# Performance work log

Measured on AMD Instinct MI355X. Metric: run time of the kernel, lower is better.

Reference implementation:

```python
import jax, jax.numpy as jnp
import numpy as np

N_ATOMS = 8192
N_PAIRS = 65536
F = 128        # n_atombasis
R = 20         # n_radialbasis
B = 5          # graph_n_blocks
EPS = 1e-8     # stability constant


def setup_inputs() -> dict:
    key = jax.random.key(0)
    ks = jax.random.split(key, 16)
    rn = lambda k, shape, s=0.05: jax.random.normal(k, shape, dtype=jnp.float32) * s
    return {
        "features": jax.random.normal(ks[0], (N_ATOMS, F), jnp.float32),
        "distances": jax.random.uniform(ks[1], (N_PAIRS,), jnp.float32, 0.5, 5.0),
        "vectors": jax.random.normal(ks[2], (N_PAIRS, 3), jnp.float32),
        "cutoffs": jax.random.uniform(ks[3], (N_PAIRS,), jnp.float32),
        "rbfs": jax.random.normal(ks[4], (N_PAIRS, R), jnp.float32),
        "filter_W": rn(ks[5], (R, B * 3 * F)),
        "filter_b": jnp.zeros((B * 3 * F,), jnp.float32),
        "int_W1": rn(ks[6], (B, F, F)),
        "int_b1": jnp.zeros((B, F), jnp.float32),
        "int_W2": rn(ks[7], (B, F, 3 * F)),
        "int_b2": jnp.zeros((B, 3 * F), jnp.float32),
        "mix_Wv": rn(ks[8], (B, F, 2 * F)),
        "mix_W1": rn(ks[9], (B, 2 * F, F)),
        "mix_b1": jnp.zeros((B, F), jnp.float32),
        "mix_W2": rn(ks[10], (B, F, 3 * F)),
        "mix_b2": jnp.zeros((B, 3 * F), jnp.float32),
        "idx_i": jax.random.randint(ks[11], (N_PAIRS,), 0, N_ATOMS),
        "idx_j": jax.random.randint(ks[12], (N_PAIRS,), 0, N_ATOMS),
    }


def reference(features, distances, vectors, cutoffs, rbfs,
              filter_W, filter_b, int_W1, int_b1, int_W2, int_b2,
              mix_Wv, mix_W1, mix_b1, mix_W2, mix_b2, idx_i, idx_j):
    n_atoms = features.shape[0]
    # Cutoff-weighted radial filters, one (3F) chunk per block: [P, B*3F]
    descriptors = (rbfs @ filter_W + filter_b) * cutoffs[:, None]
    dir_ij = vectors / distances[:, None]                       # [P, 3]

    q = features[:, None, :]                                    # [N, 1, F]
    mu = jnp.zeros((n_atoms, 3, F), dtype=features.dtype)       # [N, 3, F]

    for b in range(B):
        # --- interaction block ---
        x = jax.nn.silu(q @ int_W1[b] + int_b1[b]) @ int_W2[b] + int_b2[b]  # [N,1,3F]
        Wij = descriptors[:, None, b * 3 * F:(b + 1) * 3 * F]               # [P,1,3F]
        xj = x[idx_j] * Wij                                                 # [P,1,3F]
        muj = mu[idx_j]                                                     # [P,3,F]
        dq, dmuR, dmumu = jnp.split(xj, 3, axis=-1)                         # [P,1,F] each
        dmu = dmuR * dir_ij[:, :, None] + dmumu * muj                       # [P,3,F]
        q = q + jax.ops.segment_sum(dq, idx_i, num_segments=n_atoms)
        mu = mu + jax.ops.segment_sum(dmu, idx_i, num_segments=n_atoms)

        # --- mixing block ---
        mu_V, mu_W = jnp.split(mu @ mix_Wv[b], 2, axis=-1)                  # [N,3,F] each
        mu_Vn = jnp.sqrt(jnp.sum(mu_V ** 2, axis=-2, keepdims=True) + EPS)  # [N,1,F]
        ctx = jnp.concatenate([q, mu_Vn], axis=-1)                          # [N,1,2F]
        y = jax.nn.silu(ctx @ mix_W1[b] + mix_b1[b]) @ mix_W2[b] + mix_b2[b]
        dq_i, dmu_i, dqmu_i = jnp.split(y, 3, axis=-1)                      # [N,1,F] each
        q = q + dq_i + dqmu_i * jnp.sum(mu_V * mu_W, axis=1, keepdims=True)
        mu = mu + dmu_i * mu_W

    return q[:, 0, :], mu
```

## Files before the change

### kernel.cpp

```cpp
#include <hip/hip_runtime.h>
#include <hip/hip_bf16.h>

#define NA 8192
#define NP 65536
#define WROW 1920

typedef short short8 __attribute__((ext_vector_type(8)));
typedef short short4v __attribute__((ext_vector_type(4)));
typedef float floatx4 __attribute__((ext_vector_type(4)));

static __device__ __forceinline__ short f2bf(float f) {
    union { float f; unsigned u; } v; v.f = f;
    unsigned r = v.u + 0x7FFF + ((v.u >> 16) & 1);
    return (short)(r >> 16);
}
static __device__ __forceinline__ float bf2f(short s) {
    union { unsigned u; float f; } v;
    v.u = ((unsigned)(unsigned short)s) << 16;
    return v.f;
}
static __device__ __forceinline__ unsigned char f2fp8(float f) {
    int p = __builtin_amdgcn_cvt_pk_fp8_f32(f, 0.f, 0, false);
    return (unsigned char)(p & 0xFF);
}
static __device__ __forceinline__ float fp82f(unsigned char b) {
    return __builtin_amdgcn_cvt_f32_fp8((int)b, 0);
}
static __device__ __forceinline__ float silu(float v) {
    return v / (1.f + __expf(-v));
}

__global__ __launch_bounds__(256) void k_tconv_sw(const float* __restrict__ W,
                                                  short* __restrict__ Wt,
                                                  int K, int N, int total) {
    int idx = blockIdx.x * 256 + threadIdx.x;
    if (idx >= total) return;
    int kn = K * N;
    int b = idx / kn;
    int r = idx - b * kn;
    int tile = r >> 9;
    int li = r & 511;
    int lane = li >> 3, bb = li & 7;
    int Kt = K >> 5;
    int nt = tile / Kt, kt = tile - nt * Kt;
    int k = kt * 32 + (lane >> 4) * 8 + bb;
    int n = nt * 16 + (lane & 15);
    Wt[idx] = f2bf(W[b * kn + k * N + n]);
}

__global__ __launch_bounds__(256) void k_tconv2(const float* __restrict__ fW,
                                                short* __restrict__ fWt) {
    int idx = blockIdx.x * 256 + threadIdx.x;
    if (idx >= 5 * 12288) return;
    int b = idx / 12288;
    int r = idx - b * 12288;
    int nt = r >> 9;
    int li = r & 511;
    int lane = li >> 3, bb = li & 7;
    int k = (lane >> 4) * 8 + bb;
    int n = nt * 16 + (lane & 15);
    fWt[idx] = (k < 20) ? f2bf(fW[k * WROW + b * 384 + n]) : (short)0;
}

__global__ __launch_bounds__(256) void k_init(const float* __restrict__ feat,
                                              float* __restrict__ q,
                                              float* __restrict__ mu,
                                              short* __restrict__ q_bf,
                                              short* __restrict__ mu_bfA,
                                              int* __restrict__ counts,
                                              int* __restrict__ cursor) {
    int idx = blockIdx.x * 256 + threadIdx.x;
    if (idx < NA * 128) { float v = feat[idx]; q[idx] = v; q_bf[idx] = f2bf(v); }
    mu[idx] = 0.f;
    mu_bfA[idx] = 0;
    if (idx < NA) { counts[idx] = 0; cursor[idx] = 0; }
}

__global__ __launch_bounds__(256) void k_hist(const int* __restrict__ idx_i,
                                              int* __restrict__ counts) {
    int p = blockIdx.x * 256 + threadIdx.x;
    if (p < NP) atomicAdd(&counts[idx_i[p]], 1);
}

__global__ __launch_bounds__(1024) void k_scan(const int* __restrict__ counts,
                                               int* __restrict__ offs) {
    __shared__ int sums[1024];
    int t = threadIdx.x;
    int local[8];
    int s = 0;
    #pragma unroll
    for (int k = 0; k < 8; ++k) { local[k] = s; s += counts[t * 8 + k]; }
    sums[t] = s;
    __syncthreads();
    for (int off = 1; off < 1024; off <<= 1) {
        int v = sums[t];
        int u = (t >= off) ? sums[t - off] : 0;
        __syncthreads();
        sums[t] = v + u;
        __syncthreads();
    }
    int base = (t > 0) ? sums[t - 1] : 0;
    #pragma unroll
    for (int k = 0; k < 8; ++k) offs[t * 8 + k] = base + local[k];
    if (t == 1023) offs[NA] = sums[1023];
}

__global__ __launch_bounds__(256) void k_fill(const int* __restrict__ idx_i,
                                              const int* __restrict__ offs,
                                              int* __restrict__ cursor,
                                              int* __restrict__ plist) {
    int p = blockIdx.x * 256 + threadIdx.x;
    if (p < NP) {
        int i = idx_i[p];
        int pos = atomicAdd(&cursor[i], 1);
        plist[offs[i] + pos] = p;
    }
}

__global__ __launch_bounds__(256) void k_prep(const int* __restrict__ plist,
                                              const int* __restrict__ idx_j,
                                              const float* __restrict__ cut,
                                              const float* __restrict__ dist,
                                              const float* __restrict__ vec,
                                              const float* __restrict__ rbfs,
                                              int* __restrict__ jcsr,
                                              float* __restrict__ cut_csr,
                                              float4* __restrict__ dir_csr,
                                              short* __restrict__ rbf_c) {
    int e = blockIdx.x * 256 + threadIdx.x;
    if (e >= NP) {
        if (e < NP + 16) {
            cut_csr[e] = 0.f;
            #pragma unroll
            for (int k = 0; k < 32; ++k) rbf_c[e * 32 + k] = 0;
        }
        return;
    }
    int p = plist[e];
    jcsr[e] = idx_j[p];
    float c = cut[p];
    cut_csr[e] = c;
    float invd = 1.f / dist[p];
    float4 d;
    d.x = vec[p * 3 + 0] * invd;
    d.y = vec[p * 3 + 1] * invd;
    d.z = vec[p * 3 + 2] * invd;
    d.w = 0.f;
    dir_csr[e] = d;
    #pragma unroll
    for (int k = 0; k < 20; ++k) rbf_c[e * 32 + k] = f2bf(rbfs[p * 20 + k] * c);
    #pragma unroll
    for (int k = 20; k < 32; ++k) rbf_c[e * 32 + k] = 0;
}

__global__ __launch_bounds__(256) void k_x(const short* __restrict__ q_bf,
                                           const short* __restrict__ W1sw,
                                           const short* __restrict__ W2sw,
                                           const float* __restrict__ b1,
                                           const float* __restrict__ b2,
                                           unsigned char* __restrict__ x_fp8) {
    __shared__ __align__(16) short qtile[16 * 136];
    __shared__ __align__(16) short hs[16 * 136];
    int t = threadIdx.x;
    int wv = t >> 6, lane = t & 63, quad = lane >> 4, l16 = lane & 15;
    int a0 = blockIdx.x * 16;

    #pragma unroll
    for (int it = 0; it < 2; ++it) {
        int c = it * 256 + t;
        int row = c >> 5, col4 = c & 31;
        *(short4v*)(qtile + row * 136 + col4 * 4) =
            *(const short4v*)(q_bf + (a0 + row) * 128 + col4 * 4);
    }
    __syncthreads();

    floatx4 acc0 = {0.f, 0.f, 0.f, 0.f}, acc1 = {0.f, 0.f, 0.f, 0.f};
    #pragma unroll
    for (int kk = 0; kk < 4; ++kk) {
        short8 a  = *(const short8*)(qtile + l16 * 136 + kk * 32 + quad * 8);
        short8 b0 = *(const short8*)(W1sw + ((wv * 2 + 0) * 4 + kk) * 512 + lane * 8);
        short8 bq = *(const short8*)(W1sw + ((wv * 2 + 1) * 4 + kk) * 512 + lane * 8);
        acc0 = __builtin_amdgcn_mfma_f32_16x16x32_bf16(a, b0, acc0, 0, 0, 0);
        acc1 = __builtin_amdgcn_mfma_f32_16x16x32_bf16(a, bq, acc1, 0, 0, 0);
    }
    __syncthreads();
    {
        int n0 = wv * 32 + l16;
        float bia0 = b1[n0], bia1 = b1[n0 + 16];
        #pragma unroll
        for (int r = 0; r < 4; ++r) {
            int m = quad * 4 + r;
            hs[m * 136 + n0]      = f2bf(silu(acc0[r] + bia0));
            hs[m * 136 + n0 + 16] = f2bf(silu(acc1[r] + bia1));
        }
    }
    __syncthreads();
    floatx4 acc[6];
    #pragma unroll
    for (int jj = 0; jj < 6; ++jj) acc[jj] = {0.f, 0.f, 0.f, 0.f};
    #pragma unroll
    for (int kk = 0; kk < 4; ++kk) {
        short8 a = *(const short8*)(hs + l16 * 136 + kk * 32 + quad * 8);
        #pragma unroll
        for (int jj = 0; jj < 6; ++jj) {
            short8 b = *(const short8*)(W2sw + ((wv * 6 + jj) * 4 + kk) * 512 + lane * 8);
            acc[jj] = __builtin_amdgcn_mfma_f32_16x16x32_bf16(a, b, acc[jj], 0, 0, 0);
        }
    }
    #pragma unroll
    for (int jj = 0; jj < 6; ++jj) {
        int n = wv * 96 + jj * 16 + l16;
        float bia = b2[n];
        #pragma unroll
        for (int r = 0; r < 4; ++r) {
            int m = quad * 4 + r;
            x_fp8[(a0 + m) * 384 + n] = f2fp8(acc[jj][r] + bia);
        }
    }
}

__global__ __launch_bounds__(256, 6) void k_gather(const unsigned char* __restrict__ x_fp8,
                                                   const short* __restrict__ mu_bfA,
                                                   const short* __restrict__ rbf_c,
                                                   const short* __restrict__ fWt,
                                                   const float* __restrict__ fbp,
                                                   const int* __restrict__ jcsr,
                                                   const float* __restrict__ cut_csr,
                                                   const float4* __restrict__ dir_csr,
                                                   const int* __restrict__ offs,
                                                   float* __restrict__ q,
                                                   float* __restrict__ mu,
                                                   short* __restrict__ q_bf,
                                                   short* __restrict__ mu_bfB) {
    __shared__ short dlds[16 * 392];
    __shared__ float pm[4 * 128];
    int i = blockIdx.x;
    int t = threadIdx.x;
    int h = t >> 7;
    int f = t & 127;
    int wv = t >> 6, lane = t & 63, quad = lane >> 4, l16 = lane & 15;
    int start = offs[i], end = offs[i + 1];
    float qa = 0.f, m0a = 0.f, m1a = 0.f, m2a = 0.f;

    for (int e0 = start; e0 < end; e0 += 16) {
        if (e0 > start) __syncthreads();
        short8 a = *(const short8*)(rbf_c + (e0 + l16) * 32 + quad * 8);
        float c0 = cut_csr[e0 + quad * 4 + 0];
        float c1 = cut_csr[e0 + quad * 4 + 1];
        float c2 = cut_csr[e0 + quad * 4 + 2];
        float c3 = cut_csr[e0 + quad * 4 + 3];
        #pragma unroll
        for (int nt = 0; nt < 6; ++nt) {
            int col = wv * 96 + nt * 16 + l16;
            short8 bfr = *(const short8*)(fWt + (wv * 6 + nt) * 512 + lane * 8);
            floatx4 z = {0.f, 0.f, 0.f, 0.f};
            floatx4 acc = __builtin_amdgcn_mfma_f32_16x16x32_bf16(a, bfr, z, 0, 0, 0);
            float fbv = fbp[col];
            dlds[(quad * 4 + 0) * 392 + col] = f2bf(acc[0] + fbv * c0);
            dlds[(quad * 4 + 1) * 392 + col] = f2bf(acc[1] + fbv * c1);
            dlds[(quad * 4 + 2) * 392 + col] = f2bf(acc[2] + fbv * c2);
            dlds[(quad * 4 + 3) * 392 + col] = f2bf(acc[3] + fbv * c3);
        }
        __syncthreads();
        int lim = (end < e0 + 16) ? end : (e0 + 16);
        int e = e0 + h;
        if (e < lim) {
            int jA = jcsr[e];
            float4 dirA = dir_csr[e];
            unsigned char aX0 = x_fp8[jA * 384 + f];
            unsigned char aX1 = x_fp8[jA * 384 + 128 + f];
            unsigned char aX2 = x_fp8[jA * 384 + 256 + f];
            short aU0 = mu_bfA[jA * 384 + f];
            short aU1 = mu_bfA[jA * 384 + 128 + f];
            short aU2 = mu_bfA[jA * 384 + 256 + f];
            for (; e < lim; e += 2) {
                float x0 = fp82f(aX0), x1 = fp82f(aX1), x2 = fp82f(aX2);
                float u0 = bf2f(aU0), u1 = bf2f(aU1), u2 = bf2f(aU2);
                float4 cdir = dirA;
                int en = e + 2;
                if (en < lim) {
                    int jn = jcsr[en];
                    dirA = dir_csr[en];
                    aX0 = x_fp8[jn * 384 + f];
                    aX1 = x_fp8[jn * 384 + 128 + f];
                    aX2 = x_fp8[jn * 384 + 256 + f];
                    aU0 = mu_bfA[jn * 384 + f];
                    aU1 = mu_bfA[jn * 384 + 128 + f];
                    aU2 = mu_bfA[jn * 384 + 256 + f];
                }
                int le = e - e0;
                float wa = bf2f(dlds[le * 392 + f]);
                float wb = bf2f(dlds[le * 392 + 128 + f]);
                float wc = bf2f(dlds[le * 392 + 256 + f]);
                qa += x0 * wa;
                float xb = x1 * wb;
                float xc = x2 * wc;
                m0a += xb * cdir.x + xc * u0;
                m1a += xb * cdir.y + xc * u1;
                m2a += xb * cdir.z + xc * u2;
            }
        }
    }
    if (h == 1) {
        pm[0 * 128 + f] = qa;
        pm[1 * 128 + f] = m0a;
        pm[2 * 128 + f] = m1a;
        pm[3 * 128 + f] = m2a;
    }
    __syncthreads();
    if (h == 0) {
        qa  += pm[0 * 128 + f];
        m0a += pm[1 * 128 + f];
        m1a += pm[2 * 128 + f];
        m2a += pm[3 * 128 + f];
        float qn = q[i * 128 + f] + qa;
        q[i * 128 + f] = qn;
        q_bf[i * 128 + f] = f2bf(qn);
        float mn0 = mu[(i * 3 + 0) * 128 + f] + m0a;
        float mn1 = mu[(i * 3 + 1) * 128 + f] + m1a;
        float mn2 = mu[(i * 3 + 2) * 128 + f] + m2a;
        mu[(i * 3 + 0) * 128 + f] = mn0;
        mu[(i * 3 + 1) * 128 + f] = mn1;
        mu[(i * 3 + 2) * 128 + f] = mn2;
        mu_bfB[(i * 3 + 0) * 128 + f] = f2bf(mn0);
        mu_bfB[(i * 3 + 1) * 128 + f] = f2bf(mn1);
        mu_bfB[(i * 3 + 2) * 128 + f] = f2bf(mn2);
    }
}

__global__ __launch_bounds__(512, 4) void k_mixx(const short* __restrict__ mu_bfB,
                                                 const short* __restrict__ Wvsw,
                                                 const short* __restrict__ q_bf_ro,
                                                 const short* __restrict__ W1sw,
                                                 const short* __restrict__ W2sw,
                                                 const float* __restrict__ b1,
                                                 const float* __restrict__ b2,
                                                 float* __restrict__ q,
                                                 float* __restrict__ mu,
                                                 short* __restrict__ q_bf,
                                                 short* __restrict__ mu_bfA,
                                                 const short* __restrict__ xW1sw,
                                                 const short* __restrict__ xW2sw,
                                                 const float* __restrict__ xb1,
                                                 const float* __restrict__ xb2,
                                                 unsigned char* __restrict__ x_fp8,
                                                 int do_x) {
    __shared__ __align__(16) char smem[51968];
    short* ms    = (short*)(smem);
    short* qtile = (short*)(smem + 13056);
    short* Vv    = (short*)(smem + 17408);
    short* hs    = (short*)(smem + 17408);
    short* Vw    = (short*)(smem + 30464);
    short* vnb   = (short*)(smem + 43520);
    short* sb    = (short*)(smem + 47872);
    int t = threadIdx.x;
    int wv = t >> 6, lane = t & 63, quad = lane >> 4, l16 = lane & 15;
    int a0 = blockIdx.x * 16;

    #pragma unroll
    for (int it = 0; it < 3; ++it) {
        int c = it * 512 + t;
        int row = c >> 5, col4 = c & 31;
        *(short4v*)(ms + row * 136 + col4 * 4) =
            *(const short4v*)(mu_bfB + (a0 * 3 + row) * 128 + col4 * 4);
    }
    {
        int row = t >> 5, col4 = t & 31;
        *(short4v*)(qtile + row * 136 + col4 * 4) =
            *(const short4v*)(q_bf_ro + (a0 + row) * 128 + col4 * 4);
    }
    __syncthreads();

    {
        floatx4 acc[3][2];
        #pragma unroll
        for (int mt = 0; mt < 3; ++mt)
            #pragma unroll
            for (int nt = 0; nt < 2; ++nt) acc[mt][nt] = {0.f, 0.f, 0.f, 0.f};
        #pragma unroll
        for (int kk = 0; kk < 4; ++kk) {
            short8 a[3];
            #pragma unroll
            for (int mt = 0; mt < 3; ++mt)
                a[mt] = *(const short8*)(ms + (mt * 16 + l16) * 136 + kk * 32 + quad * 8);
            #pragma unroll
            for (int nt = 0; nt < 2; ++nt) {
                short8 b = *(const short8*)(Wvsw + ((wv * 2 + nt) * 4 + kk) * 512 + lane * 8);
                #pragma unroll
                for (int mt = 0; mt < 3; ++mt)
                    acc[mt][nt] = __builtin_amdgcn_mfma_f32_16x16x32_bf16(a[mt], b, acc[mt][nt], 0, 0, 0);
            }
        }
        __syncthreads();
        #pragma unroll
        for (int mt = 0; mt < 3; ++mt)
            #pragma unroll
            for (int nt = 0; nt < 2; ++nt)
                #pragma unroll
                for (int r = 0; r < 4; ++r) {
                    int row = mt * 16 + quad * 4 + r;
                    int col = wv * 32 + nt * 16 + l16;
                    short v = f2bf(acc[mt][nt][r]);
                    if (col < 128) Vv[row * 136 + col] = v;
                    else           Vw[row * 136 + col - 128] = v;
                }
    }
    __syncthreads();
    #pragma unroll
    for (int k = 0; k < 4; ++k) {
        int idx = k * 512 + t;
        int a = idx >> 7, c = idx & 127;
        float v0 = bf2f(Vv[(a * 3 + 0) * 136 + c]);
        float v1 = bf2f(Vv[(a * 3 + 1) * 136 + c]);
        float v2 = bf2f(Vv[(a * 3 + 2) * 136 + c]);
        float w0 = bf2f(Vw[(a * 3 + 0) * 136 + c]);
        float w1 = bf2f(Vw[(a * 3 + 1) * 136 + c]);
        float w2 = bf2f(Vw[(a * 3 + 2) * 136 + c]);
        vnb[a * 136 + c] = f2bf(sqrtf(v0 * v0 + v1 * v1 + v2 * v2 + 1e-8f));
        sb[a * 128 + c]  = f2bf(v0 * w0 + v1 * w1 + v2 * w2);
    }
    __syncthreads();
    {
        floatx4 acc0 = {0.f, 0.f, 0.f, 0.f};
        #pragma unroll
        for (int kk = 0; kk < 8; ++kk) {
            short8 a;
            if (kk < 4)
                a = *(const short8*)(qtile + l16 * 136 + kk * 32 + quad * 8);
            else
                a = *(const short8*)(vnb + l16 * 136 + (kk - 4) * 32 + quad * 8);
            short8 b0 = *(const short8*)(W1sw + (wv * 8 + kk) * 512 + lane * 8);
            acc0 = __builtin_amdgcn_mfma_f32_16x16x32_bf16(a, b0, acc0, 0, 0, 0);
        }
        __syncthreads();
        int n0 = wv * 16 + l16;
        float bia0 = b1[n0];
        #pragma unroll
        for (int r = 0; r < 4; ++r) {
            int m = quad * 4 + r;
            hs[m * 136 + n0] = f2bf(silu(acc0[r] + bia0));
        }
    }
    __syncthreads();
    {
        floatx4 accB[3];
        #pragma unroll
        for (int c = 0; c < 3; ++c) accB[c] = {0.f, 0.f, 0.f, 0.f};
        #pragma unroll
        for (int kk = 0; kk < 4; ++kk) {
            short8 a = *(const short8*)(hs + l16 * 136 + kk * 32 + quad * 8);
            #pragma unroll
            for (int c = 0; c < 3; ++c) {
                short8 b = *(const short8*)(W2sw + ((c * 8 + wv) * 4 + kk) * 512 + lane * 8);
                accB[c] = __builtin_amdgcn_mfma_f32_16x16x32_bf16(a, b, accB[c], 0, 0, 0);
            }
        }
        int co = wv * 16 + l16;
        float bq_  = b2[co];
        float bm_  = b2[128 + co];
        float bqm_ = b2[256 + co];
        #pragma unroll
        for (int r = 0; r < 4; ++r) {
            int m = quad * 4 + r;
            int ga = a0 + m;
            float dq   = accB[0][r] + bq_;
            float dmu  = accB[1][r] + bm_;
            float dqmu = accB[2][r] + bqm_;
            float sv = bf2f(sb[m * 128 + co]);
            float qn = q[ga * 128 + co] + dq + dqmu * sv;
            q[ga * 128 + co] = qn;
            short qnb = f2bf(qn);
            q_bf[ga * 128 + co] = qnb;
            qtile[m * 136 + co] = qnb;
            #pragma unroll
            for (int d = 0; d < 3; ++d) {
                float mw = bf2f(Vw[(m * 3 + d) * 136 + co]);
                float mn = mu[(ga * 3 + d) * 128 + co] + dmu * mw;
                mu[(ga * 3 + d) * 128 + co] = mn;
                mu_bfA[(ga * 3 + d) * 128 + co] = f2bf(mn);
            }
        }
    }
    if (!do_x) return;
    __syncthreads();
    {
        floatx4 acc0 = {0.f, 0.f, 0.f, 0.f};
        #pragma unroll
        for (int kk = 0; kk < 4; ++kk) {
            short8 a  = *(const short8*)(qtile + l16 * 136 + kk * 32 + quad * 8);
            short8 b0 = *(const short8*)(xW1sw + (wv * 4 + kk) * 512 + lane * 8);
            acc0 = __builtin_amdgcn_mfma_f32_16x16x32_bf16(a, b0, acc0, 0, 0, 0);
        }
        __syncthreads();
        int n0 = wv * 16 + l16;
        float bia0 = xb1[n0];
        #pragma unroll
        for (int r = 0; r < 4; ++r) {
            int m = quad * 4 + r;
            hs[m * 136 + n0] = f2bf(silu(acc0[r] + bia0));
        }
    }
    __syncthreads();
    {
        floatx4 acc[3];
        #pragma unroll
        for (int jj = 0; jj < 3; ++jj) acc[jj] = {0.f, 0.f, 0.f, 0.f};
        #pragma unroll
        for (int kk = 0; kk < 4; ++kk) {
            short8 a = *(const short8*)(hs + l16 * 136 + kk * 32 + quad * 8);
            #pragma unroll
            for (int jj = 0; jj < 3; ++jj) {
                short8 b = *(const short8*)(xW2sw + ((wv * 3 + jj) * 4 + kk) * 512 + lane * 8);
                acc[jj] = __builtin_amdgcn_mfma_f32_16x16x32_bf16(a, b, acc[jj], 0, 0, 0);
            }
        }
        #pragma unroll
        for (int jj = 0; jj < 3; ++jj) {
            int n = wv * 48 + jj * 16 + l16;
            float bia = xb2[n];
            #pragma unroll
            for (int r = 0; r < 4; ++r) {
                int m = quad * 4 + r;
                x_fp8[(a0 + m) * 384 + n] = f2fp8(acc[jj][r] + bia);
            }
        }
    }
}

extern "C" void kernel_launch(void* const* d_in, const int* in_sizes, int n_in,
                              void* d_out, int out_size, void* d_ws, size_t ws_size,
                              hipStream_t stream) {
    const float* feat = (const float*)d_in[0];
    const float* dist = (const float*)d_in[1];
    const float* vec  = (const float*)d_in[2];
    const float* cut  = (const float*)d_in[3];
    const float* rbfs = (const float*)d_in[4];
    const float* fW   = (const float*)d_in[5];
    const float* fb   = (const float*)d_in[6];
    const float* iW1  = (const float*)d_in[7];
    const float* ib1  = (const float*)d_in[8];
    const float* iW2  = (const float*)d_in[9];
    const float* ib2  = (const float*)d_in[10];
    const float* mWv  = (const float*)d_in[11];
    const float* mW1  = (const float*)d_in[12];
    const float* mb1  = (const float*)d_in[13];
    const float* mW2  = (const float*)d_in[14];
    const float* mb2  = (const float*)d_in[15];
    const int* idx_i  = (const int*)d_in[16];
    const int* idx_j  = (const int*)d_in[17];

    float* q  = (float*)d_out;
    float* mu = (float*)d_out + NA * 128;

    char* w = (char*)d_ws;
    unsigned char* x_fp8 = (unsigned char*)(w);
    short* q_bf    = (short*)(w + 6291456);
    short* mu_bfA  = (short*)(w + 8388608);
    short* mu_bfB  = (short*)(w + 14680064);
    short* W1t     = (short*)(w + 20971520);
    short* W2t     = (short*)(w + 21135360);
    short* Wvt     = (short*)(w + 21626880);
    short* mW1t    = (short*)(w + 21954560);
    short* mW2t    = (short*)(w + 22282240);
    short* fWt     = (short*)(w + 22773760);
    int*   counts  = (int*)(w + 22896640);
    int*   cursor  = (int*)(w + 22929408);
    int*   offs    = (int*)(w + 22962176);
    int*   plist   = (int*)(w + 22994960);
    int*   jcsr    = (int*)(w + 23257104);
    float* cut_csr = (float*)(w + 23519248);
    float4* dir_csr= (float4*)(w + 23781456);
    short* rbf_c   = (short*)(w + 24830032);

    k_tconv_sw<<<(5 * 16384 + 255) / 256, 256, 0, stream>>>(iW1, W1t, 128, 128, 5 * 16384);
    k_tconv_sw<<<(5 * 49152 + 255) / 256, 256, 0, stream>>>(iW2, W2t, 128, 384, 5 * 49152);
    k_tconv_sw<<<(5 * 32768 + 255) / 256, 256, 0, stream>>>(mWv, Wvt, 128, 256, 5 * 32768);
    k_tconv_sw<<<(5 * 32768 + 255) / 256, 256, 0, stream>>>(mW1, mW1t, 256, 128, 5 * 32768);
    k_tconv_sw<<<(5 * 49152 + 255) / 256, 256, 0, stream>>>(mW2, mW2t, 128, 384, 5 * 49152);
    k_tconv2<<<(5 * 12288 + 255) / 256, 256, 0, stream>>>(fW, fWt);
    k_init<<<NA * 384 / 256, 256, 0, stream>>>(feat, q, mu, q_bf, mu_bfA, counts, cursor);
    k_hist<<<NP / 256, 256, 0, stream>>>(idx_i, counts);
    k_scan<<<1, 1024, 0, stream>>>(counts, offs);
    k_fill<<<NP / 256, 256, 0, stream>>>(idx_i, offs, cursor, plist);
    k_prep<<<(NP + 16 + 255) / 256, 256, 0, stream>>>(plist, idx_j, cut, dist, vec, rbfs,
                                                      jcsr, cut_csr, dir_csr, rbf_c);

    k_x<<<NA / 16, 256, 0, stream>>>(q_bf, W1t, W2t, ib1, ib2, x_fp8);
    for (int b = 0; b < 5; ++b) {
        int bn = (b + 1) % 5;
        k_gather<<<NA, 256, 0, stream>>>(x_fp8, mu_bfA, rbf_c, fWt + b * 12288,
                                         fb + b * 384, jcsr, cut_csr, dir_csr,
                                         offs, q, mu, q_bf, mu_bfB);
        k_mixx<<<NA / 16, 512, 0, stream>>>(mu_bfB, Wvt + b * 32768, q_bf,
                                            mW1t + b * 32768, mW2t + b * 49152,
                                            mb1 + b * 128, mb2 + b * 384,
                                            q, mu, q_bf, mu_bfA,
                                            W1t + bn * 16384, W2t + bn * 49152,
                                            ib1 + bn * 128, ib2 + bn * 384,
                                            x_fp8, (b < 4) ? 1 : 0);
    }
}
```

Baseline: 442.1 us.

## Fuse setup kernels and widen per-thread gather to two features per lane

The six weight-swizzle kernels are merged into one launch, and the fill and prep kernels are merged so each pair writes its CSR slot directly, which removes the plist indirection. The padding zeroing moves into the init kernel. The gather kernel now has each wave process one edge at a time across four waves, with each lane handling two features using packed 16/32-bit loads, and the partial sums from three waves are reduced through shared memory. This cuts launch overhead and scalar byte loads, at the cost of more registers and a four-way reduction.

```diff
diff --git a/kernel.cpp b/kernel.cpp
--- a/kernel.cpp
+++ b/kernel.cpp
@@ -30,36 +30,54 @@
     return v / (1.f + __expf(-v));
 }
 
-__global__ __launch_bounds__(256) void k_tconv_sw(const float* __restrict__ W,
-                                                  short* __restrict__ Wt,
-                                                  int K, int N, int total) {
-    int idx = blockIdx.x * 256 + threadIdx.x;
-    if (idx >= total) return;
+static __device__ __forceinline__ void swz(const float* __restrict__ src,
+                                           short* __restrict__ dst,
+                                           int K, int N, int idx) {
     int kn = K * N;
     int b = idx / kn;
     int r = idx - b * kn;
-    int tile = r >> 9;
-    int li = r & 511;
+    int tile = r >> 9, li = r & 511;
     int lane = li >> 3, bb = li & 7;
     int Kt = K >> 5;
     int nt = tile / Kt, kt = tile - nt * Kt;
     int k = kt * 32 + (lane >> 4) * 8 + bb;
     int n = nt * 16 + (lane & 15);
-    Wt[idx] = f2bf(W[b * kn + k * N + n]);
-}
-
-__global__ __launch_bounds__(256) void k_tconv2(const float* __restrict__ fW,
-                                                short* __restrict__ fWt) {
+    dst[idx] = f2bf(src[b * kn + k * N + n]);
+}
+
+__global__ __launch_bounds__(256) void k_tconv_all(const float* __restrict__ iW1,
+                                                   const float* __restrict__ iW2,
+                                                   const float* __restrict__ mWv,
+                                                   const float* __restrict__ mW1,
+                                                   const float* __restrict__ mW2,
+                                                   const float* __restrict__ fW,
+                                                   short* __restrict__ W1t,
+                                                   short* __restrict__ W2t,
+                                                   short* __restrict__ Wvt,
+                                                   short* __restrict__ mW1t,
+                                                   short* __restrict__ mW2t,
+                                                   short* __restrict__ fWt) {
     int idx = blockIdx.x * 256 + threadIdx.x;
-    if (idx >= 5 * 12288) return;
-    int b = idx / 12288;
-    int r = idx - b * 12288;
-    int nt = r >> 9;
-    int li = r & 511;
-    int lane = li >> 3, bb = li & 7;
-    int k = (lane >> 4) * 8 + bb;
-    int n = nt * 16 + (lane & 15);
-    fWt[idx] = (k < 20) ? f2bf(fW[k * WROW + b * 384 + n]) : (short)0;
+    if (idx < 81920)       { swz(iW1, W1t, 128, 128, idx); return; }
+    idx -= 81920;
+    if (idx < 245760)      { swz(iW2, W2t, 128, 384, idx); return; }
+    idx -= 245760;
+    if (idx < 163840)      { swz(mWv, Wvt, 128, 256, idx); return; }
+    idx -= 163840;
+    if (idx < 163840)      { swz(mW1, mW1t, 256, 128, idx); return; }
+    idx -= 163840;
+    if (idx < 245760)      { swz(mW2, mW2t, 128, 384, idx); return; }
+    idx -= 245760;
+    if (idx < 61440) {
+        int b = idx / 12288;
+        int r = idx - b * 12288;
+        int nt = r >> 9;
+        int li = r & 511;
+        int lane = li >> 3, bb = li & 7;
+        int k = (lane >> 4) * 8 + bb;
+        int n = nt * 16 + (lane & 15);
+        fWt[idx] = (k < 20) ? f2bf(fW[k * WROW + b * 384 + n]) : (short)0;
+    }
 }
 
 __global__ __launch_bounds__(256) void k_init(const float* __restrict__ feat,
@@ -68,12 +86,19 @@
                                               short* __restrict__ q_bf,
                                               short* __restrict__ mu_bfA,
                                               int* __restrict__ counts,
-                                              int* __restrict__ cursor) {
+                                              int* __restrict__ cursor,
+                                              float* __restrict__ cut_csr,
+                                              short* __restrict__ rbf_c) {
     int idx = blockIdx.x * 256 + threadIdx.x;
     if (idx < NA * 128) { float v = feat[idx]; q[idx] = v; q_bf[idx] = f2bf(v); }
     mu[idx] = 0.f;
     mu_bfA[idx] = 0;
     if (idx < NA) { counts[idx] = 0; cursor[idx] = 0; }
+    if (idx < 16) {
+        cut_csr[NP + idx] = 0.f;
+        #pragma unroll
+        for (int k = 0; k < 32; ++k) rbf_c[(NP + idx) * 32 + k] = 0;
+    }
 }
 
 __global__ __launch_bounds__(256) void k_hist(const int* __restrict__ idx_i,
@@ -105,38 +130,23 @@
     if (t == 1023) offs[NA] = sums[1023];
 }
 
-__global__ __launch_bounds__(256) void k_fill(const int* __restrict__ idx_i,
-                                              const int* __restrict__ offs,
-                                              int* __restrict__ cursor,
-                                              int* __restrict__ plist) {
+__global__ __launch_bounds__(256) void k_fillprep(const int* __restrict__ idx_i,
+                                                  const int* __restrict__ idx_j,
+                                                  const int* __restrict__ offs,
+                                                  int* __restrict__ cursor,
+                                                  const float* __restrict__ cut,
+                                                  const float* __restrict__ dist,
+                                                  const float* __restrict__ vec,
+                                                  const float* __restrict__ rbfs,
+                                                  int* __restrict__ jcsr,
+                                                  float* __restrict__ cut_csr,
+                                                  float4* __restrict__ dir_csr,
+                                                  short* __restrict__ rbf_c) {
     int p = blockIdx.x * 256 + threadIdx.x;
-    if (p < NP) {
-        int i = idx_i[p];
-        int pos = atomicAdd(&cursor[i], 1);
-        plist[offs[i] + pos] = p;
-    }
-}
-
-__global__ __launch_bounds__(256) void k_prep(const int* __restrict__ plist,
-                                              const int* __restrict__ idx_j,
-                                              const float* __restrict__ cut,
-                                              const float* __restrict__ dist,
-                                              const float* __restrict__ vec,
-                                              const float* __restrict__ rbfs,
-                                              int* __restrict__ jcsr,
-                                              float* __restrict__ cut_csr,
-                                              float4* __restrict__ dir_csr,
-                                              short* __restrict__ rbf_c) {
-    int e = blockIdx.x * 256 + threadIdx.x;
-    if (e >= NP) {
-        if (e < NP + 16) {
-            cut_csr[e] = 0.f;
-            #pragma unroll
-            for (int k = 0; k < 32; ++k) rbf_c[e * 32 + k] = 0;
-        }
-        return;
-    }
-    int p = plist[e];
+    if (p >= NP) return;
+    int i = idx_i[p];
+    int pos = atomicAdd(&cursor[i], 1);
+    int e = offs[i] + pos;
     jcsr[e] = idx_j[p];
     float c = cut[p];
     cut_csr[e] = c;
@@ -233,14 +243,14 @@
                                                    short* __restrict__ q_bf,
                                                    short* __restrict__ mu_bfB) {
     __shared__ short dlds[16 * 392];
-    __shared__ float pm[4 * 128];
+    __shared__ float pm[3][4][128];
     int i = blockIdx.x;
     int t = threadIdx.x;
-    int h = t >> 7;
-    int f = t & 127;
     int wv = t >> 6, lane = t & 63, quad = lane >> 4, l16 = lane & 15;
+    int f2 = lane * 2;
     int start = offs[i], end = offs[i + 1];
-    float qa = 0.f, m0a = 0.f, m1a = 0.f, m2a = 0.f;
+    float qa0 = 0.f, qa1 = 0.f;
+    float m00 = 0.f, m01 = 0.f, m10 = 0.f, m11 = 0.f, m20 = 0.f, m21 = 0.f;
 
     for (int e0 = start; e0 < end; e0 += 16) {
         if (e0 > start) __syncthreads();
@@ -263,68 +273,89 @@
         }
         __syncthreads();
         int lim = (end < e0 + 16) ? end : (e0 + 16);
-        int e = e0 + h;
+        int e = e0 + wv;
         if (e < lim) {
-            int jA = jcsr[e];
+            int j = jcsr[e];
             float4 dirA = dir_csr[e];
-            unsigned char aX0 = x_fp8[jA * 384 + f];
-            unsigned char aX1 = x_fp8[jA * 384 + 128 + f];
-            unsigned char aX2 = x_fp8[jA * 384 + 256 + f];
-            short aU0 = mu_bfA[jA * 384 + f];
-            short aU1 = mu_bfA[jA * 384 + 128 + f];
-            short aU2 = mu_bfA[jA * 384 + 256 + f];
-            for (; e < lim; e += 2) {
-                float x0 = fp82f(aX0), x1 = fp82f(aX1), x2 = fp82f(aX2);
-                float u0 = bf2f(aU0), u1 = bf2f(aU1), u2 = bf2f(aU2);
+            unsigned short pX0 = *(const unsigned short*)(x_fp8 + j * 384 + f2);
+            unsigned short pX1 = *(const unsigned short*)(x_fp8 + j * 384 + 128 + f2);
+            unsigned short pX2 = *(const unsigned short*)(x_fp8 + j * 384 + 256 + f2);
+            unsigned pU0 = *(const unsigned*)(mu_bfA + (j * 3 + 0) * 128 + f2);
+            unsigned pU1 = *(const unsigned*)(mu_bfA + (j * 3 + 1) * 128 + f2);
+            unsigned pU2 = *(const unsigned*)(mu_bfA + (j * 3 + 2) * 128 + f2);
+            for (; e < lim; e += 4) {
+                unsigned short cX0 = pX0, cX1 = pX1, cX2 = pX2;
+                unsigned cU0 = pU0, cU1 = pU1, cU2 = pU2;
                 float4 cdir = dirA;
-                int en = e + 2;
+                int en = e + 4;
                 if (en < lim) {
                     int jn = jcsr[en];
                     dirA = dir_csr[en];
-                    aX0 = x_fp8[jn * 384 + f];
-                    aX1 = x_fp8[jn * 384 + 128 + f];
-                    aX2 = x_fp8[jn * 384 + 256 + f];
-                    aU0 = mu_bfA[jn * 384 + f];
-                    aU1 = mu_bfA[jn * 384 + 128 + f];
-                    aU2 = mu_bfA[jn * 384 + 256 + f];
+                    pX0 = *(const unsigned short*)(x_fp8 + jn * 384 + f2);
+                    pX1 = *(const unsigned short*)(x_fp8 + jn * 384 + 128 + f2);
+                    pX2 = *(const unsigned short*)(x_fp8 + jn * 384 + 256 + f2);
+                    pU0 = *(const unsigned*)(mu_bfA + (jn * 3 + 0) * 128 + f2);
+                    pU1 = *(const unsigned*)(mu_bfA + (jn * 3 + 1) * 128 + f2);
+                    pU2 = *(const unsigned*)(mu_bfA + (jn * 3 + 2) * 128 + f2);
                 }
                 int le = e - e0;
-                float wa = bf2f(dlds[le * 392 + f]);
-                float wb = bf2f(dlds[le * 392 + 128 + f]);
-                float wc = bf2f(dlds[le * 392 + 256 + f]);
-                qa += x0 * wa;
-                float xb = x1 * wb;
-                float xc = x2 * wc;
-                m0a += xb * cdir.x + xc * u0;
-                m1a += xb * cdir.y + xc * u1;
-                m2a += xb * cdir.z + xc * u2;
+                unsigned dA = *(const unsigned*)(dlds + le * 392 + f2);
+                unsigned dB = *(const unsigned*)(dlds + le * 392 + 128 + f2);
+                unsigned dC = *(const unsigned*)(dlds + le * 392 + 256 + f2);
+                float wa0 = bf2f((short)(dA & 0xFFFF)), wa1 = bf2f((short)(dA >> 16));
+                float wb0 = bf2f((short)(dB & 0xFFFF)), wb1 = bf2f((short)(dB >> 16));
+                float wc0 = bf2f((short)(dC & 0xFFFF)), wc1 = bf2f((short)(dC >> 16));
+                qa0 += fp82f((unsigned char)(cX0 & 0xFF)) * wa0;
+                qa1 += fp82f((unsigned char)(cX0 >> 8)) * wa1;
+                float xb0 = fp82f((unsigned char)(cX1 & 0xFF)) * wb0;
+                float xb1 = fp82f((unsigned char)(cX1 >> 8)) * wb1;
+                float xc0 = fp82f((unsigned char)(cX2 & 0xFF)) * wc0;
+                float xc1 = fp82f((unsigned char)(cX2 >> 8)) * wc1;
+                m00 += xb0 * cdir.x + xc0 * bf2f((short)(cU0 & 0xFFFF));
+                m01 += xb1 * cdir.x + xc1 * bf2f((short)(cU0 >> 16));
+                m10 += xb0 * cdir.y + xc0 * bf2f((short)(cU1 & 0xFFFF));
+                m11 += xb1 * cdir.y + xc1 * bf2f((short)(cU1 >> 16));
+                m20 += xb0 * cdir.z + xc0 * bf2f((short)(cU2 & 0xFFFF));
+                m21 += xb1 * cdir.z + xc1 * bf2f((short)(cU2 >> 16));
             }
         }
     }
-    if (h == 1) {
-        pm[0 * 128 + f] = qa;
-        pm[1 * 128 + f] = m0a;
-        pm[2 * 128 + f] = m1a;
-        pm[3 * 128 + f] = m2a;
-    }
-    __syncthreads();
-    if (h == 0) {
-        qa  += pm[0 * 128 + f];
-        m0a += pm[1 * 128 + f];
-        m1a += pm[2 * 128 + f];
-        m2a += pm[3 * 128 + f];
-        float qn = q[i * 128 + f] + qa;
-        q[i * 128 + f] = qn;
-        q_bf[i * 128 + f] = f2bf(qn);
-        float mn0 = mu[(i * 3 + 0) * 128 + f] + m0a;
-        float mn1 = mu[(i * 3 + 1) * 128 + f] + m1a;
-        float mn2 = mu[(i * 3 + 2) * 128 + f] + m2a;
-        mu[(i * 3 + 0) * 128 + f] = mn0;
-        mu[(i * 3 + 1) * 128 + f] = mn1;
-        mu[(i * 3 + 2) * 128 + f] = mn2;
-        mu_bfB[(i * 3 + 0) * 128 + f] = f2bf(mn0);
-        mu_bfB[(i * 3 + 1) * 128 + f] = f2bf(mn1);
-        mu_bfB[(i * 3 + 2) * 128 + f] = f2bf(mn2);
+    if (wv > 0) {
+        pm[wv - 1][0][f2] = qa0; pm[wv - 1][0][f2 + 1] = qa1;
+        pm[wv - 1][1][f2] = m00; pm[wv - 1][1][f2 + 1] = m01;
+        pm[wv - 1][2][f2] = m10; pm[wv - 1][2][f2 + 1] = m11;
+        pm[wv - 1][3][f2] = m20; pm[wv - 1][3][f2 + 1] = m21;
+    }
+    __syncthreads();
+    if (wv == 0) {
+        #pragma unroll
+        for (int s = 0; s < 3; ++s) {
+            qa0 += pm[s][0][f2]; qa1 += pm[s][0][f2 + 1];
+            m00 += pm[s][1][f2]; m01 += pm[s][1][f2 + 1];
+            m10 += pm[s][2][f2]; m11 += pm[s][2][f2 + 1];
+            m20 += pm[s][3][f2]; m21 += pm[s][3][f2 + 1];
+        }
+        float2 qv = *(const float2*)(q + i * 128 + f2);
+        qv.x += qa0; qv.y += qa1;
+        *(float2*)(q + i * 128 + f2) = qv;
+        unsigned qb = (unsigned)(unsigned short)f2bf(qv.x) |
+                      ((unsigned)(unsigned short)f2bf(qv.y) << 16);
+        *(unsigned*)(q_bf + i * 128 + f2) = qb;
+        float2 m0 = *(const float2*)(mu + (i * 3 + 0) * 128 + f2);
+        float2 m1 = *(const float2*)(mu + (i * 3 + 1) * 128 + f2);
+        float2 m2 = *(const float2*)(mu + (i * 3 + 2) * 128 + f2);
+        m0.x += m00; m0.y += m01;
+        m1.x += m10; m1.y += m11;
+        m2.x += m20; m2.y += m21;
+        *(float2*)(mu + (i * 3 + 0) * 128 + f2) = m0;
+        *(float2*)(mu + (i * 3 + 1) * 128 + f2) = m1;
+        *(float2*)(mu + (i * 3 + 2) * 128 + f2) = m2;
+        *(unsigned*)(mu_bfB + (i * 3 + 0) * 128 + f2) =
+            (unsigned)(unsigned short)f2bf(m0.x) | ((unsigned)(unsigned short)f2bf(m0.y) << 16);
+        *(unsigned*)(mu_bfB + (i * 3 + 1) * 128 + f2) =
+            (unsigned)(unsigned short)f2bf(m1.x) | ((unsigned)(unsigned short)f2bf(m1.y) << 16);
+        *(unsigned*)(mu_bfB + (i * 3 + 2) * 128 + f2) =
+            (unsigned)(unsigned short)f2bf(m2.x) | ((unsigned)(unsigned short)f2bf(m2.y) << 16);
     }
 }
 
@@ -566,24 +597,19 @@
     int*   counts  = (int*)(w + 22896640);
     int*   cursor  = (int*)(w + 22929408);
     int*   offs    = (int*)(w + 22962176);
-    int*   plist   = (int*)(w + 22994960);
     int*   jcsr    = (int*)(w + 23257104);
     float* cut_csr = (float*)(w + 23519248);
     float4* dir_csr= (float4*)(w + 23781456);
     short* rbf_c   = (short*)(w + 24830032);
 
-    k_tconv_sw<<<(5 * 16384 + 255) / 256, 256, 0, stream>>>(iW1, W1t, 128, 128, 5 * 16384);
-    k_tconv_sw<<<(5 * 49152 + 255) / 256, 256, 0, stream>>>(iW2, W2t, 128, 384, 5 * 49152);
-    k_tconv_sw<<<(5 * 32768 + 255) / 256, 256, 0, stream>>>(mWv, Wvt, 128, 256, 5 * 32768);
-    k_tconv_sw<<<(5 * 32768 + 255) / 256, 256, 0, stream>>>(mW1, mW1t, 256, 128, 5 * 32768);
-    k_tconv_sw<<<(5 * 49152 + 255) / 256, 256, 0, stream>>>(mW2, mW2t, 128, 384, 5 * 49152);
-    k_tconv2<<<(5 * 12288 + 255) / 256, 256, 0, stream>>>(fW, fWt);
-    k_init<<<NA * 384 / 256, 256, 0, stream>>>(feat, q, mu, q_bf, mu_bfA, counts, cursor);
+    k_tconv_all<<<(962560 + 255) / 256, 256, 0, stream>>>(iW1, iW2, mWv, mW1, mW2, fW,
+                                                          W1t, W2t, Wvt, mW1t, mW2t, fWt);
+    k_init<<<NA * 384 / 256, 256, 0, stream>>>(feat, q, mu, q_bf, mu_bfA, counts, cursor,
+                                               cut_csr, rbf_c);
     k_hist<<<NP / 256, 256, 0, stream>>>(idx_i, counts);
     k_scan<<<1, 1024, 0, stream>>>(counts, offs);
-    k_fill<<<NP / 256, 256, 0, stream>>>(idx_i, offs, cursor, plist);
-    k_prep<<<(NP + 16 + 255) / 256, 256, 0, stream>>>(plist, idx_j, cut, dist, vec, rbfs,
-                                                      jcsr, cut_csr, dir_csr, rbf_c);
+    k_fillprep<<<NP / 256, 256, 0, stream>>>(idx_i, idx_j, offs, cursor, cut, dist, vec,
+                                             rbfs, jcsr, cut_csr, dir_csr, rbf_c);
 
     k_x<<<NA / 16, 256, 0, stream>>>(q_bf, W1t, W2t, ib1, ib2, x_fp8);
     for (int b = 0; b < 5; ++b) {
```

Measured after the change: 511.2 us. +15.6%, slower.
